# Kernel optimization log

Hardware: AMD Instinct MI355X
Metric: run time of the kernel (lower is better)

## Reference

```python
import jax, jax.numpy as jnp
import numpy as np
from math import sqrt

D, H, B, L = 1024, 16, 2, 2048
DK = D // H

def linear(x, w, b):
    # torch Linear layout: w (out, in)
    return x @ w.T + b

def conv1d(x, w, b, padding, groups=1):
    # x: (B, C, L); w: (O, I/groups, K) -> torch Conv1d semantics
    y = jax.lax.conv_general_dilated(
        x, w, window_strides=(1,), padding=(padding,),
        dimension_numbers=('NCH', 'OIH', 'NCH'), feature_group_count=groups)
    return y + b[None, :, None]

def setup_inputs() -> dict:
    key = jax.random.key(0)
    ks = jax.random.split(key, 26)
    def n(k, shape, s=0.02):
        return jax.random.normal(k, shape, jnp.float32) * s
    return {
        'x': jax.random.normal(ks[0], (B, L, D), jnp.float32),
        'Wq_w': n(ks[1], (D, D)), 'Wq_b': n(ks[2], (D,)),
        'Wk_w': n(ks[3], (D, D)), 'Wk_b': n(ks[4], (D,)),
        'Wv_w': n(ks[5], (D, D)), 'Wv_b': n(ks[6], (D,)),
        'convq_w': n(ks[7], (D, D, 3)), 'convq_b': n(ks[8], (D,)),
        'convk_w': n(ks[9], (D, D, 3)), 'convk_b': n(ks[10], (D,)),
        'qproj_w': n(ks[11], (D, 2 * D)), 'qproj_b': n(ks[12], (D,)),
        'kproj_w': n(ks[13], (D, 2 * D)), 'kproj_b': n(ks[14], (D,)),
        'tau1_w': n(ks[15], (2 * D, 1, 3)), 'tau1_b': n(ks[16], (2 * D,)),
        'tau2_w': n(ks[17], (H, 2 * D, 1)), 'tau2_b': n(ks[18], (H,)),
        'del1_w': n(ks[19], (2 * D, 1, 3)), 'del1_b': n(ks[20], (2 * D,)),
        'del2_w': n(ks[21], (H, 2 * D, 1)), 'del2_b': n(ks[22], (H,)),
        'out_w': n(ks[23], (D, D)), 'out_b': n(ks[24], (D,)),
    }

def reference(x, Wq_w, Wq_b, Wk_w, Wk_b, Wv_w, Wv_b,
              convq_w, convq_b, convk_w, convk_b,
              qproj_w, qproj_b, kproj_w, kproj_b,
              tau1_w, tau1_b, tau2_w, tau2_b,
              del1_w, del1_b, del2_w, del2_b,
              out_w, out_b):
    b_, l_, _ = x.shape

    # Q branch: linear -> conv3 -> concat -> proj
    q_in = linear(x, Wq_w, Wq_b).transpose(0, 2, 1)          # (B, D, L)
    Q3 = conv1d(q_in, convq_w, convq_b, (1, 1))              # (B, D, L)
    Q_cat = jnp.concatenate([q_in, Q3], axis=1).transpose(0, 2, 1)  # (B, L, 2D)
    Q = linear(Q_cat, qproj_w, qproj_b).reshape(b_, l_, H, DK).transpose(0, 2, 1, 3)

    # K branch
    k_in = linear(x, Wk_w, Wk_b).transpose(0, 2, 1)
    K3 = conv1d(k_in, convk_w, convk_b, (1, 1))
    K_cat = jnp.concatenate([k_in, K3], axis=1).transpose(0, 2, 1)
    K = linear(K_cat, kproj_w, kproj_b).reshape(b_, l_, H, DK).transpose(0, 2, 1, 3)

    V = linear(x, Wv_w, Wv_b).reshape(b_, l_, H, DK).transpose(0, 2, 1, 3)

    # per-head tau (query-row scale) and delta (key-column bias), shape (B, H, L)
    x_conv = x.transpose(0, 2, 1)                             # (B, D, L)
    tau = jax.nn.sigmoid(conv1d(
        jax.nn.gelu(conv1d(x_conv, tau1_w, tau1_b, (1, 1), groups=D), approximate=False),
        tau2_w, tau2_b, (0, 0)))
    delta = jax.nn.sigmoid(conv1d(
        jax.nn.gelu(conv1d(x_conv, del1_w, del1_b, (1, 1), groups=D), approximate=False),
        del2_w, del2_b, (0, 0)))

    scores = jnp.einsum('bhqd,bhkd->bhqk', Q, K) / sqrt(DK)   # (B, H, L, L)
    scores = scores * tau[..., None] + delta[:, :, None, :]
    attn = jax.nn.softmax(scores, axis=-1)                    # dropout = identity (eval)
    out = jnp.einsum('bhqk,bhkd->bhqd', attn, V)
    out = out.transpose(0, 2, 1, 3).reshape(b_, l_, D)
    return linear(out, out_w, out_b)
```

## Files before the change

kernel.cpp:

```cpp
#include <hip/hip_runtime.h>

typedef __bf16 bf16_t;
typedef __bf16 bf16x8 __attribute__((ext_vector_type(8)));
typedef __bf16 bf16x4 __attribute__((ext_vector_type(4)));
typedef float f32x4 __attribute__((ext_vector_type(4)));
typedef unsigned uint2v __attribute__((ext_vector_type(2)));

__device__ __forceinline__ void gload_lds16(const bf16_t* g, bf16_t* l) {
  __builtin_amdgcn_global_load_lds(
      (__attribute__((address_space(1))) void*)g,
      (__attribute__((address_space(3))) void*)l, 16, 0, 0);
}

__global__ void k_detect(const unsigned int* __restrict__ xw, int* __restrict__ flag) {
  __shared__ int red[256];
  int c = 0;
  for (int j = 0; j < 16; ++j) {
    unsigned int w = xw[threadIdx.x + (j << 8)];
    unsigned int e = (w >> 7) & 0xFF;
    c += (e >= 100 && e <= 150) ? 1 : 0;
  }
  red[threadIdx.x] = c;
  __syncthreads();
  for (int s = 128; s > 0; s >>= 1) {
    if (threadIdx.x < s) red[threadIdx.x] += red[threadIdx.x + s];
    __syncthreads();
  }
  if (threadIdx.x == 0) flag[0] = (red[0] > 2048) ? 1 : 0;
}

__device__ __constant__ long c_offs[26] = {
    0, 4194304, 4195328, 4196352, 4197376, 4198400, 4199424, 6296576,
    6297600, 8394752, 8395776, 8401920, 8403968, 8436736, 8436752,
    8442896, 8444944, 8477712, 8477728,
    0, 1048576, 2097152, 3145728,
    0, 1048576, 1049600};
struct CanonArgs { const void* src[18]; };

__global__ void k_canon(CanonArgs a, int base, int n, const int* __restrict__ flag,
                        bf16_t* __restrict__ dst) {
  long e0 = ((long)blockIdx.x * 256 + threadIdx.x) * 8;
  if (e0 >= c_offs[base + n]) return;
  int k = 0;
  while (e0 >= c_offs[base + k + 1]) ++k;
  const long rel = e0 - c_offs[base + k];
  if (flag[0]) {
    *(bf16x8*)&dst[e0] = *(const bf16x8*)((const bf16_t*)a.src[k] + rel);
  } else {
    const float* sf = (const float*)a.src[k] + rel;
    f32x4 lo = *(const f32x4*)sf;
    f32x4 hi = *(const f32x4*)(sf + 4);
    bf16x8 o;
    o[0] = (bf16_t)lo[0]; o[1] = (bf16_t)lo[1]; o[2] = (bf16_t)lo[2]; o[3] = (bf16_t)lo[3];
    o[4] = (bf16_t)hi[0]; o[5] = (bf16_t)hi[1]; o[6] = (bf16_t)hi[2]; o[7] = (bf16_t)hi[3];
    *(bf16x8*)&dst[e0] = o;
  }
}

__global__ void k_zero_pads(bf16_t* __restrict__ pad, bf16_t* __restrict__ zvec) {
  int idx = blockIdx.x * 256 + threadIdx.x;
  if (idx < 1024) zvec[idx] = (bf16_t)0.0f;
  if (idx >= 8192) return;
  int b = idx >> 11;
  int r = (idx >> 10) & 1;
  int c = idx & 1023;
  long row = (long)b * 2050 + (r ? 2049 : 0);
  pad[row * 1024 + c] = (bf16_t)0.0f;
}

__global__ __launch_bounds__(256) void k_ctT(
    const void* __restrict__ wq, const void* __restrict__ wk,
    bf16_t* __restrict__ dq, bf16_t* __restrict__ dk,
    const int* __restrict__ flag) {
  __shared__ bf16_t T[64][72];
  int blk = blockIdx.x;
  const int br = blk >= 768;
  if (br) blk -= 768;
  const void* w = br ? wk : wq;
  bf16_t* dst = br ? dk : dq;
  const int ot = blk / 48, jt = blk - ot * 48;
  const int o0 = ot << 6, j0 = jt << 6;
  const int t = threadIdx.x;
  const int f = flag[0];
#pragma unroll
  for (int it = 0; it < 2; ++it) {
    const int ch = t + (it << 8);
    const int r = ch >> 3, c8 = (ch & 7) << 3;
    const long off = (long)(o0 + r) * 3072 + j0 + c8;
    if (f) {
      *(bf16x8*)&T[r][c8] = *(const bf16x8*)((const bf16_t*)w + off);
    } else {
      const float* sf = (const float*)w + off;
      bf16x8 o8;
#pragma unroll
      for (int e = 0; e < 8; ++e) o8[e] = (bf16_t)sf[e];
      *(bf16x8*)&T[r][c8] = o8;
    }
  }
  __syncthreads();
  const int j = t >> 2, oc0 = (t & 3) << 4;
  const int jj = j0 + j;
  const int drow = (jj % 3) * 1024 + jj / 3;
  bf16_t* dp = dst + (long)drow * 1024 + o0 + oc0;
#pragma unroll
  for (int s = 0; s < 16; ++s) dp[s] = T[oc0 + s][j];
}

__global__ void k_addwp1(bf16_t* __restrict__ Hq, bf16_t* __restrict__ Hk,
                         const bf16_t* __restrict__ qp, const bf16_t* __restrict__ kp) {
  const long e0 = ((long)blockIdx.x * 256 + threadIdx.x) * 8;
  if (e0 >= 2097152L) return;
  const int br = (int)(e0 >> 20);
  const int rem = (int)(e0 & 1048575);
  const int o = rem >> 10, i = rem & 1023;
  bf16_t* h = (br ? Hk : Hq) + (long)o * 3072 + 1024 + i;
  const bf16_t* w = (br ? kp : qp) + (long)o * 2048 + i;
  bf16x8 a = *(const bf16x8*)h;
  bf16x8 b = *(const bf16x8*)w;
  bf16x8 r;
#pragma unroll
  for (int e = 0; e < 8; ++e) r[e] = (bf16_t)((float)a[e] + (float)b[e]);
  *(bf16x8*)h = r;
}

__global__ __launch_bounds__(256) void k_bvec(
    const bf16_t* __restrict__ qp, const bf16_t* __restrict__ kp,
    const bf16_t* __restrict__ cqb, const bf16_t* __restrict__ ckb,
    const bf16_t* __restrict__ qpb, const bf16_t* __restrict__ kpb,
    bf16_t* __restrict__ bvec) {
  const int idx = blockIdx.x * 256 + threadIdx.x;
  if (idx >= 2048) return;
  const int br = idx >> 10, o = idx & 1023;
  const bf16_t* wrow = (br ? kp : qp) + (long)o * 2048 + 1024;
  const bf16_t* cb = br ? ckb : cqb;
  float s = 0.f;
  for (int m8 = 0; m8 < 1024; m8 += 8) {
    bf16x8 w8 = *(const bf16x8*)&wrow[m8];
    bf16x8 c8 = *(const bf16x8*)&cb[m8];
#pragma unroll
    for (int e = 0; e < 8; ++e) s += (float)w8[e] * (float)c8[e];
  }
  bvec[idx] = (bf16_t)(s + (float)((br ? kpb : qpb)[o]));
}

struct GemmP {
  const bf16_t *A0;
  const bf16_t *B0, *B1, *B2;
  const bf16_t *bias0, *bias1, *bias2;
  bf16_t *C0, *C1, *C2;
  long a_jump, at_jump;
  long cj0, cj1, cj2, ct_jump;
  long b_jump;
  int rpb, rpt, lda, ldb, bsel_by_n, bshift, K, csel_by_n;
  int crs0, ccs0, crs1, ccs1, crs2, ccs2;
};

template <int BN, int BK, bool FINAL>
__global__ __launch_bounds__(256) void k_gemm(GemmP p, const int* __restrict__ flagp) {
  __shared__ __align__(16) bf16_t As[2][128 * BK];
  __shared__ __align__(16) bf16_t Bs[2][BN * BK];
  constexpr int CPR = BK / 8;
  const int tid = threadIdx.x;
  const int gx = gridDim.x;
  int lin = blockIdx.y * gx + blockIdx.x;
  const int nwg = gx * gridDim.y;
  lin = ((lin & 7) * (nwg >> 3)) + (lin >> 3);
  const int n0 = (lin % gx) * BN;
  const int m0 = (lin / gx) << 7;
  const int batch = m0 / p.rpb;
  const int tap = (m0 - batch * p.rpb) / p.rpt;
  const int bidx = p.bsel_by_n ? (n0 >> 10) : (m0 >> p.bshift);
  const bf16_t* Bp = p.b_jump ? (p.B0 + (long)bidx * p.b_jump)
                              : (bidx == 0 ? p.B0 : (bidx == 1 ? p.B1 : p.B2));
  const bf16_t* biasp = bidx == 0 ? p.bias0 : (bidx == 1 ? p.bias1 : p.bias2);
  const long abase = (long)batch * p.a_jump + (long)tap * p.at_jump;
  const int wid = tid >> 6, lane = tid & 63;
  const int l15 = lane & 15, lg = lane >> 4;
  const int nloc = n0 & 1023;

  constexpr int MI = (BN == 128) ? 4 : 2;
  const int wr = (BN == 128) ? ((wid >> 1) << 6) : (wid << 5);
  const int wc = (BN == 128) ? ((wid & 1) << 6) : 0;
  const int l15sw = (l15 >> 1) & (CPR - 1);

  f32x4 acc[MI][4];
#pragma unroll
  for (int i = 0; i < MI; ++i)
#pragma unroll
    for (int j = 0; j < 4; ++j) acc[i][j] = (f32x4){0.f, 0.f, 0.f, 0.f};

  auto stage = [&](int bufi, int k) {
#pragma unroll
    for (int it = 0; it < (128 * CPR) / 256; ++it) {
      const int c = it * 256 + tid;
      const int row = c / CPR, kc = c % CPR;
      const int kg = k + ((kc ^ ((row >> 1) & (CPR - 1))) << 3);
      gload_lds16(p.A0 + abase + (long)(m0 + row) * p.lda + kg, &As[bufi][c << 3]);
    }
#pragma unroll
    for (int it = 0; it < (BN * CPR) / 256; ++it) {
      const int c = it * 256 + tid;
      const int row = c / CPR, kc = c % CPR;
      const int kg = k + ((kc ^ ((row >> 1) & (CPR - 1))) << 3);
      gload_lds16(Bp + (long)(nloc + row) * p.ldb + kg, &Bs[bufi][c << 3]);
    }
  };

  const int nk = p.K / BK;
  int buf = 0;
  stage(0, 0);
  asm volatile("s_waitcnt vmcnt(0)" ::: "memory");
  __builtin_amdgcn_s_barrier();
  __builtin_amdgcn_sched_barrier(0);
  for (int kt = 0; kt < nk; ++kt) {
    if (kt + 1 < nk) stage(buf ^ 1, (kt + 1) * BK);
#pragma unroll
    for (int kh = 0; kh < BK / 32; ++kh) {
      bf16x8 af[MI], bfr[4];
      const int csw = (((kh << 2) | lg) ^ l15sw) << 3;
#pragma unroll
      for (int i = 0; i < MI; ++i)
        af[i] = *(const bf16x8*)&As[buf][(wr + (i << 4) + l15) * BK + csw];
#pragma unroll
      for (int j = 0; j < 4; ++j)
        bfr[j] = *(const bf16x8*)&Bs[buf][(wc + (j << 4) + l15) * BK + csw];
#pragma unroll
      for (int i = 0; i < MI; ++i)
#pragma unroll
        for (int j = 0; j < 4; ++j)
          acc[i][j] = __builtin_amdgcn_mfma_f32_16x16x32_bf16(af[i], bfr[j], acc[i][j], 0, 0, 0);
    }
    if (kt + 1 < nk) asm volatile("s_waitcnt vmcnt(0)" ::: "memory");
    __builtin_amdgcn_s_barrier();
    __builtin_amdgcn_sched_barrier(0);
    buf ^= 1;
  }

  const int cp = p.csel_by_n ? (n0 >> 10) : (m0 >> p.bshift);
  bf16_t* Cb = cp == 0 ? p.C0 : (cp == 1 ? p.C1 : p.C2);
  const int crs = cp == 0 ? p.crs0 : (cp == 1 ? p.crs1 : p.crs2);
  const int ccs = cp == 0 ? p.ccs0 : (cp == 1 ? p.ccs1 : p.ccs2);
  const long cj = cp == 0 ? p.cj0 : (cp == 1 ? p.cj1 : p.cj2);
  const bool f32out = FINAL && (flagp[0] == 0);
  const long cbase = (long)batch * cj + (long)tap * p.ct_jump;
#pragma unroll
  for (int i = 0; i < MI; ++i) {
    const int row = m0 + wr + (i << 4) + (lg << 2);
#pragma unroll
    for (int j = 0; j < 4; ++j) {
      const int col = nloc + wc + (j << 4) + l15;
      const float bv = (float)biasp[col];
#pragma unroll
      for (int r = 0; r < 4; ++r) {
        const float val = acc[i][j][r] + bv;
        const long ci = cbase + (long)(row + r) * crs + (long)col * ccs;
        if (FINAL && f32out) ((float*)Cb)[ci] = val;
        else Cb[ci] = (bf16_t)val;
      }
    }
  }
}

__global__ __launch_bounds__(256) void k_taudelta(
    const bf16_t* __restrict__ x,
    const bf16_t* __restrict__ t1w, const bf16_t* __restrict__ t1b,
    const bf16_t* __restrict__ t2w, const bf16_t* __restrict__ t2b,
    const bf16_t* __restrict__ d1w, const bf16_t* __restrict__ d1b,
    const bf16_t* __restrict__ d2w, const bf16_t* __restrict__ d2b,
    float* __restrict__ tau, float* __restrict__ dlt)
{
  const int bt = blockIdx.x;
  const int t = bt & 2047;
  const int b = bt >> 11;
  const int tid = threadIdx.x;
  const bf16_t* xr = x + ((long)bt << 10);

  float acc[32];
#pragma unroll
  for (int i = 0; i < 32; ++i) acc[i] = 0.f;

  for (int j = 0; j < 8; ++j) {
    const int c = tid + (j << 8);
    const int src = c >> 1;
    const float x0 = (float)xr[src];
    const float xm = (t > 0) ? (float)xr[src - 1024] : 0.f;
    const float xp = (t < 2047) ? (float)xr[src + 1024] : 0.f;
    float st = (float)t1w[3 * c] * xm + (float)t1w[3 * c + 1] * x0 +
               (float)t1w[3 * c + 2] * xp + (float)t1b[c];
    float sd = (float)d1w[3 * c] * xm + (float)d1w[3 * c + 1] * x0 +
               (float)d1w[3 * c + 2] * xp + (float)d1b[c];
    const float gt = 0.5f * st * (1.f + erff(st * 0.70710678118f));
    const float gd = 0.5f * sd * (1.f + erff(sd * 0.70710678118f));
#pragma unroll
    for (int h = 0; h < 16; ++h) {
      acc[h]      += (float)t2w[(h << 11) + c] * gt;
      acc[16 + h] += (float)d2w[(h << 11) + c] * gd;
    }
  }

  __shared__ float red[256][33];
  __shared__ float red2[8][32];
#pragma unroll
  for (int i = 0; i < 32; ++i) red[tid][i] = acc[i];
  __syncthreads();
  const int i = tid & 31, g = tid >> 5;
  float p = 0.f;
#pragma unroll
  for (int k2 = 0; k2 < 32; ++k2) p += red[(g << 5) + k2][i];
  __syncthreads();
  red2[g][i] = p;
  __syncthreads();
  if (tid < 32) {
    float s = 0.f;
#pragma unroll
    for (int g2 = 0; g2 < 8; ++g2) s += red2[g2][tid];
    const int h = tid & 15;
    if (tid < 16) {
      s += (float)t2b[h];
      tau[((long)((b << 4) + h) << 11) + t] = 1.f / (1.f + __expf(-s));
    } else {
      s += (float)d2b[h];
      dlt[((long)((b << 4) + h) << 11) + t] =
          1.4426950408889634f / (1.f + __expf(-s));
    }
  }
}

__device__ __forceinline__ unsigned pk2(float a, float b) {
  union { bf16_t h[2]; unsigned u; } z;
  z.h[0] = (bf16_t)a; z.h[1] = (bf16_t)b;
  return z.u;
}

__global__ __launch_bounds__(256) void k_attn(
    const bf16_t* __restrict__ QKb, const bf16_t* __restrict__ VT,
    const float* __restrict__ tau, const float* __restrict__ dlt,
    bf16_t* __restrict__ O)
{
  const int lin = blockIdx.x;
  const int wg = ((lin & 7) << 7) + (lin >> 3);
  const int bh = wg >> 5, qt = wg & 31;
  const int tid = threadIdx.x;
  const int lane = tid & 63;
  const int wid = tid >> 6;
  const int l15 = lane & 15, lg = lane >> 4;
  const int b = bh >> 4, h = bh & 15;
  const int qbase = (qt << 6) + (wid << 4);

  const bf16_t* Qp = QKb + ((long)b << 21) + (h << 6);
  const bf16_t* Kp = QKb + 4194304 + ((long)b << 21) + (h << 6);
  const bf16_t* Vp = VT + ((long)bh << 17);

  __shared__ __align__(16) bf16_t Ks[2][4096];
  __shared__ __align__(16) bf16_t Vs[2][4096];
  __shared__ unsigned Plds[4][16][32];

  bf16x8 qf[2];
#pragma unroll
  for (int kd = 0; kd < 2; ++kd)
    qf[kd] = *(const bf16x8*)&Qp[((long)(qbase + l15) << 10) + (kd << 5) + (lg << 3)];
  const float tq = tau[((long)bh << 11) + qbase + l15] * (0.125f * 1.4426950408889634f);

  bf16x8 onesf;
#pragma unroll
  for (int e = 0; e < 8; ++e) onesf[e] = (bf16_t)1.0f;

  f32x4 accO[4];
#pragma unroll
  for (int d = 0; d < 4; ++d) accO[d] = (f32x4){0.f, 0.f, 0.f, 0.f};
  f32x4 accL = (f32x4){0.f, 0.f, 0.f, 0.f};

  const int xr = (l15 & 7) << 2;
  const int c0 = ((lg ^ (l15 & 7)) << 3);
  const int c1 = (((4 | lg) ^ (l15 & 7)) << 3);
  const int rowb = l15 << 6;
  const int sK_r0 = tid >> 3, sK_c0 = ((tid & 7) ^ (sK_r0 & 7)) << 3;
  const int sK_r1 = (tid + 256) >> 3, sK_c1 = (((tid + 256) & 7) ^ (sK_r1 & 7)) << 3;
  const bf16_t* kb0 = Kp + ((long)sK_r0 << 10) + sK_c0;
  const bf16_t* kb1 = Kp + ((long)sK_r1 << 10) + sK_c1;
  const bf16_t* vb0 = Vp + ((long)sK_r0 << 11) + sK_c0;
  const bf16_t* vb1 = Vp + ((long)sK_r1 << 11) + sK_c1;
  bf16_t* ldK0[2] = {&Ks[0][tid << 3], &Ks[1][tid << 3]};
  bf16_t* ldK1[2] = {&Ks[0][(tid + 256) << 3], &Ks[1][(tid + 256) << 3]};
  bf16_t* ldV0[2] = {&Vs[0][tid << 3], &Vs[1][tid << 3]};
  bf16_t* ldV1[2] = {&Vs[0][(tid + 256) << 3], &Vs[1][(tid + 256) << 3]};
  const float* dlp = dlt + ((long)bh << 11) + (lg << 2);

  auto stageKV = [&](int bufi, int kk) {
    gload_lds16(kb0 + ((long)kk << 10), ldK0[bufi]);
    gload_lds16(kb1 + ((long)kk << 10), ldK1[bufi]);
    gload_lds16(vb0 + kk, ldV0[bufi]);
    gload_lds16(vb1 + kk, ldV1[bufi]);
  };

  int buf = 0;
  stageKV(0, 0);
  asm volatile("s_waitcnt vmcnt(0)" ::: "memory");
  __builtin_amdgcn_s_barrier();
  __builtin_amdgcn_sched_barrier(0);

  for (int kk = 0; kk < 2048; kk += 64) {
    if (kk + 64 < 2048) stageKV(buf ^ 1, kk + 64);

    f32x4 st[4];
    __builtin_amdgcn_s_setprio(1);
#pragma unroll
    for (int kb = 0; kb < 4; ++kb) {
      const int rk = (kb << 10) + rowb;
      f32x4 z = (f32x4){0.f, 0.f, 0.f, 0.f};
      z = __builtin_amdgcn_mfma_f32_16x16x32_bf16(
          *(const bf16x8*)&Ks[buf][rk + c0], qf[0], z, 0, 0, 0);
      z = __builtin_amdgcn_mfma_f32_16x16x32_bf16(
          *(const bf16x8*)&Ks[buf][rk + c1], qf[1], z, 0, 0, 0);
      st[kb] = z;
    }
    __builtin_amdgcn_s_setprio(0);

#pragma unroll
    for (int kb = 0; kb < 4; ++kb) {
      const f32x4 dl = *(const f32x4*)(dlp + kk + (kb << 4));
      const float p0 = exp2f(fmaf(st[kb][0], tq, dl[0]));
      const float p1 = exp2f(fmaf(st[kb][1], tq, dl[1]));
      const float p2 = exp2f(fmaf(st[kb][2], tq, dl[2]));
      const float p3 = exp2f(fmaf(st[kb][3], tq, dl[3]));
      uint2v pp;
      pp[0] = pk2(p0, p1);
      pp[1] = pk2(p2, p3);
      *(uint2v*)&Plds[wid][l15][((kb << 3) + (lg << 1)) ^ xr] = pp;
    }
    asm volatile("s_waitcnt lgkmcnt(0)" ::: "memory");
    __builtin_amdgcn_sched_barrier(0);
    const bf16x8 pf0 = *(const bf16x8*)&Plds[wid][l15][(lg << 2) ^ xr];
    const bf16x8 pf1 = *(const bf16x8*)&Plds[wid][l15][(16 | (lg << 2)) ^ xr];
    asm volatile("s_waitcnt lgkmcnt(0)" ::: "memory");
    __builtin_amdgcn_sched_barrier(0);

    __builtin_amdgcn_s_setprio(1);
#pragma unroll
    for (int d = 0; d < 4; ++d) {
      const int rv = (d << 10) + rowb;
      accO[d] = __builtin_amdgcn_mfma_f32_16x16x32_bf16(
          *(const bf16x8*)&Vs[buf][rv + c0], pf0, accO[d], 0, 0, 0);
      accO[d] = __builtin_amdgcn_mfma_f32_16x16x32_bf16(
          *(const bf16x8*)&Vs[buf][rv + c1], pf1, accO[d], 0, 0, 0);
    }
    accL = __builtin_amdgcn_mfma_f32_16x16x32_bf16(onesf, pf0, accL, 0, 0, 0);
    accL = __builtin_amdgcn_mfma_f32_16x16x32_bf16(onesf, pf1, accL, 0, 0, 0);
    __builtin_amdgcn_s_setprio(0);

    if (kk + 64 < 2048) asm volatile("s_waitcnt vmcnt(0)" ::: "memory");
    __builtin_amdgcn_s_barrier();
    __builtin_amdgcn_sched_barrier(0);
    buf ^= 1;
  }

  bf16_t* Ob = O + ((long)b << 21) + (h << 6);
  const float inv = 1.f / accL[0];
#pragma unroll
  for (int d = 0; d < 4; ++d) {
    bf16x4 ov;
#pragma unroll
    for (int r = 0; r < 4; ++r) ov[r] = (bf16_t)(accO[d][r] * inv);
    *(bf16x4*)&Ob[((long)(qbase + l15) << 10) + (d << 4) + (lg << 2)] = ov;
  }
}

extern "C" void kernel_launch(void* const* d_in, const int* in_sizes, int n_in,
                              void* d_out, int out_size, void* d_ws, size_t ws_size,
                              hipStream_t stream) {
  char* w = (char*)d_ws;
  int* flag     = (int*)w;
  bf16_t* canon = (bf16_t*)(w + 16);
  bf16_t* pad   = (bf16_t*)(w + 16955472);
  bf16_t* swq   = (bf16_t*)(w + 33749072);
  bf16_t* cvout = (bf16_t*)(w + 40040528);
  bf16_t* QKb   = (bf16_t*)(w + 48429136);
  bf16_t* VT    = (bf16_t*)(w + 65206352);

  bf16_t* xc      = canon;
  bf16_t* Wq_b    = canon + 4194304;
  bf16_t* Wk_b    = canon + 4195328;
  bf16_t* Wv_b    = canon + 4196352;
  bf16_t* convq_b = canon + 4197376;
  bf16_t* convk_b = canon + 4198400;
  bf16_t* qproj_w = canon + 4199424;
  bf16_t* qproj_b = canon + 6296576;
  bf16_t* kproj_w = canon + 6297600;
  bf16_t* kproj_b = canon + 8394752;
  bf16_t* tau1_w  = canon + 8395776;
  bf16_t* tau1_b  = canon + 8401920;
  bf16_t* tau2_w  = canon + 8403968;
  bf16_t* tau2_b  = canon + 8436736;
  bf16_t* del1_w  = canon + 8436752;
  bf16_t* del1_b  = canon + 8442896;
  bf16_t* del2_w  = canon + 8444944;
  bf16_t* del2_b  = canon + 8477712;

  bf16_t* pad_q = pad;
  bf16_t* Wq_w = swq, *Wk_w = swq + 1048576, *Wv_w = swq + 2097152;
  float* tau = (float*)swq;
  float* dlt = (float*)((char*)swq + 262144);
  bf16_t* bvec = (bf16_t*)((char*)swq + 524288);
  bf16_t* zvec = (bf16_t*)((char*)swq + 528384);
  bf16_t* ctT_q = QKb;
  bf16_t* ctT_k = QKb + 3145728;
  bf16_t* Hq = cvout;
  bf16_t* Hk = xc;
  const long hk_delta = (long)(Hk - Hq);
  bf16_t* outw_bf = pad;
  bf16_t* outb_bf = pad + 1048576;
  bf16_t* attn_out = xc;

  k_detect<<<1, 256, 0, stream>>>((const unsigned int*)d_in[0], flag);

  CanonArgs ca{};
  {
    const int idxA[18] = {0, 2, 4, 6, 8, 10, 11, 12, 13, 14,
                          15, 16, 17, 18, 19, 20, 21, 22};
    for (int i = 0; i < 18; ++i) ca.src[i] = d_in[idxA[i]];
    k_canon<<<4140, 256, 0, stream>>>(ca, 0, 18, flag, canon);
  }
  {
    CanonArgs cw{};
    cw.src[0] = d_in[1]; cw.src[1] = d_in[3]; cw.src[2] = d_in[5];
    k_canon<<<1536, 256, 0, stream>>>(cw, 19, 3, flag, swq);
  }
  k_zero_pads<<<32, 256, 0, stream>>>(pad, zvec);

  {
    GemmP p{};
    p.A0 = xc;
    p.B0 = Wq_w; p.B1 = Wk_w; p.B2 = Wv_w;
    p.bias0 = Wq_b; p.bias1 = Wk_b; p.bias2 = Wv_b;
    p.C0 = pad_q + 1024; p.C1 = pad_q + 4198400 + 1024; p.C2 = VT;
    p.a_jump = 0; p.at_jump = 0;
    p.cj0 = 2048; p.cj1 = 2048; p.cj2 = 2095104; p.ct_jump = 0;
    p.b_jump = 0;
    p.rpb = 2048; p.rpt = 1 << 30; p.lda = 1024; p.ldb = 1024;
    p.bsel_by_n = 1; p.bshift = 12; p.K = 1024; p.csel_by_n = 1;
    p.crs0 = 1024; p.ccs0 = 1; p.crs1 = 1024; p.ccs1 = 1; p.crs2 = 1; p.ccs2 = 2048;
    k_gemm<128, 32, false><<<dim3(24, 32), 256, 0, stream>>>(p, flag);
  }

  k_taudelta<<<4096, 256, 0, stream>>>(xc, tau1_w, tau1_b, tau2_w, tau2_b,
                                       del1_w, del1_b, del2_w, del2_b, tau, dlt);

  k_ctT<<<1536, 256, 0, stream>>>(d_in[7], d_in[9], ctT_q, ctT_k, flag);

  {
    GemmP p{};
    p.A0 = qproj_w + 1024;
    p.B0 = ctT_q; p.B1 = ctT_q; p.B2 = ctT_q;
    p.bias0 = p.bias1 = p.bias2 = zvec;
    p.C0 = p.C1 = p.C2 = Hq;
    p.a_jump = (long)(kproj_w - qproj_w) - 3072L * 2048;
    p.at_jump = -2097152;
    p.cj0 = p.cj1 = p.cj2 = hk_delta - 9437184;
    p.ct_jump = -3144704;
    p.b_jump = 1048576;
    p.rpb = 3072; p.rpt = 1024; p.lda = 2048; p.ldb = 1024;
    p.bsel_by_n = 0; p.bshift = 10; p.K = 1024; p.csel_by_n = 0;
    p.crs0 = p.crs1 = p.crs2 = 3072; p.ccs0 = p.ccs1 = p.ccs2 = 1;
    k_gemm<128, 64, false><<<dim3(8, 48), 256, 0, stream>>>(p, flag);
  }

  k_addwp1<<<1024, 256, 0, stream>>>(Hq, Hk, qproj_w, kproj_w);
  k_bvec<<<8, 256, 0, stream>>>(qproj_w, kproj_w, convq_b, convk_b,
                                qproj_b, kproj_b, bvec);

  {
    GemmP p{};
    p.A0 = pad;
    p.B0 = Hq; p.B1 = Hk; p.B2 = Hk;
    p.bias0 = bvec; p.bias1 = bvec + 1024; p.bias2 = bvec + 1024;
    p.C0 = p.C1 = p.C2 = QKb;
    p.a_jump = 4096; p.at_jump = 2048;
    p.cj0 = p.cj1 = p.cj2 = 0; p.ct_jump = 0;
    p.b_jump = 0;
    p.rpb = 4096; p.rpt = 2048; p.lda = 1024; p.ldb = 3072;
    p.bsel_by_n = 0; p.bshift = 12; p.K = 3072; p.csel_by_n = 0;
    p.crs0 = p.crs1 = p.crs2 = 1024; p.ccs0 = p.ccs1 = p.ccs2 = 1;
    k_gemm<128, 64, false><<<dim3(8, 64), 256, 0, stream>>>(p, flag);
  }

  {
    CanonArgs co{};
    co.src[0] = d_in[23]; co.src[1] = d_in[24];
    k_canon<<<513, 256, 0, stream>>>(co, 23, 2, flag, outw_bf);
  }

  k_attn<<<1024, 256, 0, stream>>>(QKb, VT, tau, dlt, attn_out);

  {
    GemmP p{};
    p.A0 = attn_out;
    p.B0 = p.B1 = p.B2 = outw_bf;
    p.bias0 = p.bias1 = p.bias2 = outb_bf;
    p.C0 = p.C1 = p.C2 = (bf16_t*)d_out;
    p.a_jump = 0; p.at_jump = 0;
    p.cj0 = p.cj1 = p.cj2 = 0; p.ct_jump = 0;
    p.b_jump = 0;
    p.rpb = 1 << 30; p.rpt = 1 << 30; p.lda = 1024; p.ldb = 1024;
    p.bsel_by_n = 0; p.bshift = 12; p.K = 1024; p.csel_by_n = 0;
    p.crs0 = p.crs1 = p.crs2 = 1024; p.ccs0 = p.ccs1 = p.ccs2 = 1;
    k_gemm<64, 32, true><<<dim3(16, 32), 256, 0, stream>>>(p, flag);
  }
}
```

Measured before the change: 378.5 us.

## Stage 128 keys per barrier in attention and merge prep kernels

The attention kernel now stages two 64-key K/V tiles per pipeline step into four LDS buffers. It processes both before one wait and barrier, which halves the synchronisation points per key sweep. This raises LDS use per block from about 40KB to about 72KB, which can lower how many blocks fit on a CU. Separately, the weight-add and bias-vector prep kernels are merged into a single launch to save one kernel launch.

Result: slower. 406.5 us (+7.4%).

```diff
diff --git a/kernel.cpp b/kernel.cpp
--- a/kernel.cpp
+++ b/kernel.cpp
@@ -106,41 +106,41 @@
   for (int s = 0; s < 16; ++s) dp[s] = T[oc0 + s][j];
 }
 
-__global__ void k_addwp1(bf16_t* __restrict__ Hq, bf16_t* __restrict__ Hk,
-                         const bf16_t* __restrict__ qp, const bf16_t* __restrict__ kp) {
-  const long e0 = ((long)blockIdx.x * 256 + threadIdx.x) * 8;
-  if (e0 >= 2097152L) return;
-  const int br = (int)(e0 >> 20);
-  const int rem = (int)(e0 & 1048575);
-  const int o = rem >> 10, i = rem & 1023;
-  bf16_t* h = (br ? Hk : Hq) + (long)o * 3072 + 1024 + i;
-  const bf16_t* w = (br ? kp : qp) + (long)o * 2048 + i;
-  bf16x8 a = *(const bf16x8*)h;
-  bf16x8 b = *(const bf16x8*)w;
-  bf16x8 r;
-#pragma unroll
-  for (int e = 0; e < 8; ++e) r[e] = (bf16_t)((float)a[e] + (float)b[e]);
-  *(bf16x8*)h = r;
-}
-
-__global__ __launch_bounds__(256) void k_bvec(
+__global__ __launch_bounds__(256) void k_prep2(
+    bf16_t* __restrict__ Hq, bf16_t* __restrict__ Hk,
     const bf16_t* __restrict__ qp, const bf16_t* __restrict__ kp,
     const bf16_t* __restrict__ cqb, const bf16_t* __restrict__ ckb,
     const bf16_t* __restrict__ qpb, const bf16_t* __restrict__ kpb,
     bf16_t* __restrict__ bvec) {
-  const int idx = blockIdx.x * 256 + threadIdx.x;
-  if (idx >= 2048) return;
-  const int br = idx >> 10, o = idx & 1023;
-  const bf16_t* wrow = (br ? kp : qp) + (long)o * 2048 + 1024;
-  const bf16_t* cb = br ? ckb : cqb;
-  float s = 0.f;
-  for (int m8 = 0; m8 < 1024; m8 += 8) {
-    bf16x8 w8 = *(const bf16x8*)&wrow[m8];
-    bf16x8 c8 = *(const bf16x8*)&cb[m8];
-#pragma unroll
-    for (int e = 0; e < 8; ++e) s += (float)w8[e] * (float)c8[e];
-  }
-  bvec[idx] = (bf16_t)(s + (float)((br ? kpb : qpb)[o]));
+  if (blockIdx.x < 1024) {
+    const long e0 = ((long)blockIdx.x * 256 + threadIdx.x) * 8;
+    if (e0 >= 2097152L) return;
+    const int br = (int)(e0 >> 20);
+    const int rem = (int)(e0 & 1048575);
+    const int o = rem >> 10, i = rem & 1023;
+    bf16_t* hh = (br ? Hk : Hq) + (long)o * 3072 + 1024 + i;
+    const bf16_t* ww = (br ? kp : qp) + (long)o * 2048 + i;
+    bf16x8 a = *(const bf16x8*)hh;
+    bf16x8 b2 = *(const bf16x8*)ww;
+    bf16x8 r;
+#pragma unroll
+    for (int e = 0; e < 8; ++e) r[e] = (bf16_t)((float)a[e] + (float)b2[e]);
+    *(bf16x8*)hh = r;
+  } else {
+    const int idx = (blockIdx.x - 1024) * 256 + threadIdx.x;
+    if (idx >= 2048) return;
+    const int br = idx >> 10, o = idx & 1023;
+    const bf16_t* wrow = (br ? kp : qp) + (long)o * 2048 + 1024;
+    const bf16_t* cb = br ? ckb : cqb;
+    float s = 0.f;
+    for (int m8 = 0; m8 < 1024; m8 += 8) {
+      bf16x8 w8 = *(const bf16x8*)&wrow[m8];
+      bf16x8 c8 = *(const bf16x8*)&cb[m8];
+#pragma unroll
+      for (int e = 0; e < 8; ++e) s += (float)w8[e] * (float)c8[e];
+    }
+    bvec[idx] = (bf16_t)(s + (float)((br ? kpb : qpb)[o]));
+  }
 }
 
 struct GemmP {
@@ -351,8 +351,8 @@
   const bf16_t* Kp = QKb + 4194304 + ((long)b << 21) + (h << 6);
   const bf16_t* Vp = VT + ((long)bh << 17);
 
-  __shared__ __align__(16) bf16_t Ks[2][4096];
-  __shared__ __align__(16) bf16_t Vs[2][4096];
+  __shared__ __align__(16) bf16_t Ks[4][4096];
+  __shared__ __align__(16) bf16_t Vs[4][4096];
   __shared__ unsigned Plds[4][16][32];
 
   bf16x8 qf[2];
@@ -380,17 +380,17 @@
   const bf16_t* kb1 = Kp + ((long)sK_r1 << 10) + sK_c1;
   const bf16_t* vb0 = Vp + ((long)sK_r0 << 11) + sK_c0;
   const bf16_t* vb1 = Vp + ((long)sK_r1 << 11) + sK_c1;
-  bf16_t* ldK0[2] = {&Ks[0][tid << 3], &Ks[1][tid << 3]};
-  bf16_t* ldK1[2] = {&Ks[0][(tid + 256) << 3], &Ks[1][(tid + 256) << 3]};
-  bf16_t* ldV0[2] = {&Vs[0][tid << 3], &Vs[1][tid << 3]};
-  bf16_t* ldV1[2] = {&Vs[0][(tid + 256) << 3], &Vs[1][(tid + 256) << 3]};
   const float* dlp = dlt + ((long)bh << 11) + (lg << 2);
 
+  auto stageHalf = [&](int idx, int kk2) {
+    gload_lds16(kb0 + ((long)kk2 << 10), &Ks[idx][tid << 3]);
+    gload_lds16(kb1 + ((long)kk2 << 10), &Ks[idx][(tid + 256) << 3]);
+    gload_lds16(vb0 + kk2, &Vs[idx][tid << 3]);
+    gload_lds16(vb1 + kk2, &Vs[idx][(tid + 256) << 3]);
+  };
   auto stageKV = [&](int bufi, int kk) {
-    gload_lds16(kb0 + ((long)kk << 10), ldK0[bufi]);
-    gload_lds16(kb1 + ((long)kk << 10), ldK1[bufi]);
-    gload_lds16(vb0 + kk, ldV0[bufi]);
-    gload_lds16(vb1 + kk, ldV1[bufi]);
+    stageHalf(bufi << 1, kk);
+    stageHalf((bufi << 1) | 1, kk + 64);
   };
 
   int buf = 0;
@@ -399,56 +399,62 @@
   __builtin_amdgcn_s_barrier();
   __builtin_amdgcn_sched_barrier(0);
 
-  for (int kk = 0; kk < 2048; kk += 64) {
-    if (kk + 64 < 2048) stageKV(buf ^ 1, kk + 64);
-
-    f32x4 st[4];
-    __builtin_amdgcn_s_setprio(1);
-#pragma unroll
-    for (int kb = 0; kb < 4; ++kb) {
-      const int rk = (kb << 10) + rowb;
-      f32x4 z = (f32x4){0.f, 0.f, 0.f, 0.f};
-      z = __builtin_amdgcn_mfma_f32_16x16x32_bf16(
-          *(const bf16x8*)&Ks[buf][rk + c0], qf[0], z, 0, 0, 0);
-      z = __builtin_amdgcn_mfma_f32_16x16x32_bf16(
-          *(const bf16x8*)&Ks[buf][rk + c1], qf[1], z, 0, 0, 0);
-      st[kb] = z;
-    }
-    __builtin_amdgcn_s_setprio(0);
-
-#pragma unroll
-    for (int kb = 0; kb < 4; ++kb) {
-      const f32x4 dl = *(const f32x4*)(dlp + kk + (kb << 4));
-      const float p0 = exp2f(fmaf(st[kb][0], tq, dl[0]));
-      const float p1 = exp2f(fmaf(st[kb][1], tq, dl[1]));
-      const float p2 = exp2f(fmaf(st[kb][2], tq, dl[2]));
-      const float p3 = exp2f(fmaf(st[kb][3], tq, dl[3]));
-      uint2v pp;
-      pp[0] = pk2(p0, p1);
-      pp[1] = pk2(p2, p3);
-      *(uint2v*)&Plds[wid][l15][((kb << 3) + (lg << 1)) ^ xr] = pp;
-    }
-    asm volatile("s_waitcnt lgkmcnt(0)" ::: "memory");
-    __builtin_amdgcn_sched_barrier(0);
-    const bf16x8 pf0 = *(const bf16x8*)&Plds[wid][l15][(lg << 2) ^ xr];
-    const bf16x8 pf1 = *(const bf16x8*)&Plds[wid][l15][(16 | (lg << 2)) ^ xr];
-    asm volatile("s_waitcnt lgkmcnt(0)" ::: "memory");
-    __builtin_amdgcn_sched_barrier(0);
-
-    __builtin_amdgcn_s_setprio(1);
-#pragma unroll
-    for (int d = 0; d < 4; ++d) {
-      const int rv = (d << 10) + rowb;
-      accO[d] = __builtin_amdgcn_mfma_f32_16x16x32_bf16(
-          *(const bf16x8*)&Vs[buf][rv + c0], pf0, accO[d], 0, 0, 0);
-      accO[d] = __builtin_amdgcn_mfma_f32_16x16x32_bf16(
-          *(const bf16x8*)&Vs[buf][rv + c1], pf1, accO[d], 0, 0, 0);
-    }
-    accL = __builtin_amdgcn_mfma_f32_16x16x32_bf16(onesf, pf0, accL, 0, 0, 0);
-    accL = __builtin_amdgcn_mfma_f32_16x16x32_bf16(onesf, pf1, accL, 0, 0, 0);
-    __builtin_amdgcn_s_setprio(0);
-
-    if (kk + 64 < 2048) asm volatile("s_waitcnt vmcnt(0)" ::: "memory");
+  for (int kk = 0; kk < 2048; kk += 128) {
+    if (kk + 128 < 2048) stageKV(buf ^ 1, kk + 128);
+
+#pragma unroll
+    for (int half = 0; half < 2; ++half) {
+      const int ti = (buf << 1) | half;
+      const int kо = kk + (half << 6);
+
+      f32x4 st[4];
+      __builtin_amdgcn_s_setprio(1);
+#pragma unroll
+      for (int kb = 0; kb < 4; ++kb) {
+        const int rk = (kb << 10) + rowb;
+        f32x4 z = (f32x4){0.f, 0.f, 0.f, 0.f};
+        z = __builtin_amdgcn_mfma_f32_16x16x32_bf16(
+            *(const bf16x8*)&Ks[ti][rk + c0], qf[0], z, 0, 0, 0);
+        z = __builtin_amdgcn_mfma_f32_16x16x32_bf16(
+            *(const bf16x8*)&Ks[ti][rk + c1], qf[1], z, 0, 0, 0);
+        st[kb] = z;
+      }
+      __builtin_amdgcn_s_setprio(0);
+
+#pragma unroll
+      for (int kb = 0; kb < 4; ++kb) {
+        const f32x4 dl = *(const f32x4*)(dlp + kо + (kb << 4));
+        const float p0 = exp2f(fmaf(st[kb][0], tq, dl[0]));
+        const float p1 = exp2f(fmaf(st[kb][1], tq, dl[1]));
+        const float p2 = exp2f(fmaf(st[kb][2], tq, dl[2]));
+        const float p3 = exp2f(fmaf(st[kb][3], tq, dl[3]));
+        uint2v pp;
+        pp[0] = pk2(p0, p1);
+        pp[1] = pk2(p2, p3);
+        *(uint2v*)&Plds[wid][l15][((kb << 3) + (lg << 1)) ^ xr] = pp;
+      }
+      asm volatile("s_waitcnt lgkmcnt(0)" ::: "memory");
+      __builtin_amdgcn_sched_barrier(0);
+      const bf16x8 pf0 = *(const bf16x8*)&Plds[wid][l15][(lg << 2) ^ xr];
+      const bf16x8 pf1 = *(const bf16x8*)&Plds[wid][l15][(16 | (lg << 2)) ^ xr];
+      asm volatile("s_waitcnt lgkmcnt(0)" ::: "memory");
+      __builtin_amdgcn_sched_barrier(0);
+
+      __builtin_amdgcn_s_setprio(1);
+#pragma unroll
+      for (int d = 0; d < 4; ++d) {
+        const int rv = (d << 10) + rowb;
+        accO[d] = __builtin_amdgcn_mfma_f32_16x16x32_bf16(
+            *(const bf16x8*)&Vs[ti][rv + c0], pf0, accO[d], 0, 0, 0);
+        accO[d] = __builtin_amdgcn_mfma_f32_16x16x32_bf16(
+            *(const bf16x8*)&Vs[ti][rv + c1], pf1, accO[d], 0, 0, 0);
+      }
+      accL = __builtin_amdgcn_mfma_f32_16x16x32_bf16(onesf, pf0, accL, 0, 0, 0);
+      accL = __builtin_amdgcn_mfma_f32_16x16x32_bf16(onesf, pf1, accL, 0, 0, 0);
+      __builtin_amdgcn_s_setprio(0);
+    }
+
+    if (kk + 128 < 2048) asm volatile("s_waitcnt vmcnt(0)" ::: "memory");
     __builtin_amdgcn_s_barrier();
     __builtin_amdgcn_sched_barrier(0);
     buf ^= 1;
@@ -564,9 +570,8 @@
     k_gemm<128, 64, false><<<dim3(8, 48), 256, 0, stream>>>(p, flag);
   }
 
-  k_addwp1<<<1024, 256, 0, stream>>>(Hq, Hk, qproj_w, kproj_w);
-  k_bvec<<<8, 256, 0, stream>>>(qproj_w, kproj_w, convq_b, convk_b,
-                                qproj_b, kproj_b, bvec);
+  k_prep2<<<1032, 256, 0, stream>>>(Hq, Hk, qproj_w, kproj_w,
+                                    convq_b, convk_b, qproj_b, kproj_b, bvec);
 
   {
     GemmP p{};
```
